# Optimization experiments

Hardware: AMD Instinct MI355X
Metric: run time of the kernel (lower is better)

The kernel has to match this reference:

```python
import jax, jax.numpy as jnp
import numpy as np
from jax import lax

T, H, L = 4096, 1024, 2  # seq_len, hidden (=input_dim), num_layers


def setup_inputs() -> dict:
    key = jax.random.key(0)
    ks = jax.random.split(key, 12)
    s = 1.0 / np.sqrt(H)
    u = lambda k, shp: jax.random.uniform(k, shp, jnp.float32, -s, s)
    return {
        "x": jax.random.normal(ks[0], (T, 1, H), jnp.float32),
        # encoder LSTM params, stacked over layers: W_ih/W_hh [L,4H,H], biases [L,4H]
        "enc_W_ih": u(ks[1], (L, 4 * H, H)),
        "enc_W_hh": u(ks[2], (L, 4 * H, H)),
        "enc_b_ih": u(ks[3], (L, 4 * H)),
        "enc_b_hh": u(ks[4], (L, 4 * H)),
        # decoder LSTM params
        "dec_W_ih": u(ks[5], (L, 4 * H, H)),
        "dec_W_hh": u(ks[6], (L, 4 * H, H)),
        "dec_b_ih": u(ks[7], (L, 4 * H)),
        "dec_b_hh": u(ks[8], (L, 4 * H)),
        # output Linear: H -> input_dim (=H)
        "out_W": u(ks[9], (H, H)),
        "out_b": u(ks[10], (H,)),
    }


def _lstm_layer(x_seq, W_ih, W_hh, b_ih, b_hh, h0, c0):
    """One LSTM layer over a full sequence. x_seq: [T,1,I]; returns hs [T,1,H], hT, cT [1,H].
    PyTorch gate order: i, f, g, o."""
    # precompute input contributions for all steps (one big GEMM)
    xg = jnp.einsum('tbi,gi->tbg', x_seq, W_ih) + b_ih  # [T,1,4H]

    def step(carry, xg_t):
        h, c = carry
        g = xg_t + h @ W_hh.T + b_hh  # [1,4H]
        i, f, gg, o = jnp.split(g, 4, axis=-1)
        c = jax.nn.sigmoid(f) * c + jax.nn.sigmoid(i) * jnp.tanh(gg)
        h = jax.nn.sigmoid(o) * jnp.tanh(c)
        return (h, c), h

    (hT, cT), hs = lax.scan(step, (h0, c0), xg)
    return hs, hT, cT


def reference(x, enc_W_ih, enc_W_hh, enc_b_ih, enc_b_hh,
              dec_W_ih, dec_W_hh, dec_b_ih, dec_b_hh, out_W, out_b):
    Tn = x.shape[0]
    nH = enc_W_hh.shape[-1]
    nL = enc_W_ih.shape[0]
    z = jnp.zeros((1, nH), x.dtype)

    # ---- encoder: stacked LSTM, layer-sequential (eval mode: no dropout) ----
    seq = x
    enc_h, enc_c = [], []
    for l in range(nL):
        seq, hT, cT = _lstm_layer(seq, enc_W_ih[l], enc_W_hh[l], enc_b_ih[l], enc_b_hh[l], z, z)
        enc_h.append(hT)
        enc_c.append(cT)

    final_hidden = seq[-1:]  # [1,1,H] = encoded_output[-1].unsqueeze(0)

    # ---- decoder: same constant input fed every step; init state = encoder (h,c) ----
    # The torch loop runs the full stacked LSTM one step at a time with constant input x;
    # stacked LSTMs are layer-separable, so we run each layer over all T steps at once.
    dseq = jnp.broadcast_to(final_hidden, (Tn, 1, nH))
    for l in range(nL):
        dseq, _, _ = _lstm_layer(dseq, dec_W_ih[l], dec_W_hh[l], dec_b_ih[l], dec_b_hh[l], enc_h[l], enc_c[l])

    out = jnp.einsum('tbh,oh->tbo', dseq, out_W) + out_b
    out = jnp.where(out > 0, out, 0.01 * out)  # LeakyReLU(0.01)
    reconstructed = jnp.flip(out, axis=0)  # decoded.reverse()
    return reconstructed, final_hidden
```

## Files before the change

kernel.cpp:

```cpp
#include <hip/hip_runtime.h>
#include <stdint.h>


#define T_STEPS 4096
#define H_DIM   1024
#define SLOT_U64 1024
#define SLOT_DW  2048
#define NSLOT   4097
#define M1 0x7E57u
#define M2 0x7E58u
#define PANIC_ITERS (1u<<25)

using u32 = uint32_t;
using u64 = unsigned long long;

static __device__ __forceinline__ float sigf(float x){ return 1.0f/(1.0f+__expf(-x)); }
static __device__ __forceinline__ float tanh_f(float x){
  x = fminf(20.f, fmaxf(-20.f, x));
  float e = __expf(-2.f*x);
  return (1.f-e)/(1.f+e);
}

static __device__ __forceinline__ bool tag_ok(u64 v, u32 magic){
  return ((((u32)(v>>16))&0xFFFFu)==magic) & (((u32)(v>>48))==magic);
}
static __device__ __forceinline__ float untag1(u64 v){
  return __uint_as_float( (((u32)v)&0xFFFFu) | (((u32)(v>>32))<<16) );
}
static __device__ __forceinline__ u64 tag1(u32 magic, float h){
  u32 b=__float_as_uint(h);
  u64 lo = (u64)((magic<<16)|(b&0xFFFFu));
  u64 hi = ((u64)((magic<<16)|(b>>16)))<<32;
  return hi|lo;
}

static __device__ __forceinline__ void poll_h2(const u64* __restrict__ q,
                                               u32 magic, float* dst,
                                               u32* panic){
  u64 v0=0,v1=0; bool ok0=false,ok1=false; u32 it=0;
  for(;;){
    if(!ok0) v0=__hip_atomic_load(q,  __ATOMIC_RELAXED,__HIP_MEMORY_SCOPE_AGENT);
    if(!ok1) v1=__hip_atomic_load(q+1,__ATOMIC_RELAXED,__HIP_MEMORY_SCOPE_AGENT);
    ok0 = ok0 || tag_ok(v0,magic);
    ok1 = ok1 || tag_ok(v1,magic);
    if(ok0 & ok1) break;
    ++it;
    if((it & 255u)==0u){
      if(__hip_atomic_load(panic,__ATOMIC_RELAXED,__HIP_MEMORY_SCOPE_AGENT)==0xDEADBEEFu) break;
      if(it>PANIC_ITERS){ __hip_atomic_store(panic,0xDEADBEEFu,__ATOMIC_RELAXED,__HIP_MEMORY_SCOPE_AGENT); break; }
    }
    __builtin_amdgcn_s_sleep(4);
  }
  dst[0]=untag1(v0);
  dst[1]=untag1(v1);
}

static __device__ __forceinline__ void poll_in2h2(const u64* __restrict__ qa, u32 mA,
                                                  const u64* __restrict__ qb, u32 mB,
                                                  float* da, float* db, u32* panic){
  u64 a0=0,a1=0,b0=0,b1=0; bool oa0=false,oa1=false,ob0=false,ob1=false; u32 it=0;
  for(;;){
    if(!oa0) a0=__hip_atomic_load(qa,  __ATOMIC_RELAXED,__HIP_MEMORY_SCOPE_AGENT);
    if(!oa1) a1=__hip_atomic_load(qa+1,__ATOMIC_RELAXED,__HIP_MEMORY_SCOPE_AGENT);
    if(!ob0) b0=__hip_atomic_load(qb,  __ATOMIC_RELAXED,__HIP_MEMORY_SCOPE_AGENT);
    if(!ob1) b1=__hip_atomic_load(qb+1,__ATOMIC_RELAXED,__HIP_MEMORY_SCOPE_AGENT);
    oa0 = oa0 || tag_ok(a0,mA);
    oa1 = oa1 || tag_ok(a1,mA);
    ob0 = ob0 || tag_ok(b0,mB);
    ob1 = ob1 || tag_ok(b1,mB);
    if(oa0 & oa1 & ob0 & ob1) break;
    ++it;
    if((it & 255u)==0u){
      if(__hip_atomic_load(panic,__ATOMIC_RELAXED,__HIP_MEMORY_SCOPE_AGENT)==0xDEADBEEFu) break;
      if(it>PANIC_ITERS){ __hip_atomic_store(panic,0xDEADBEEFu,__ATOMIC_RELAXED,__HIP_MEMORY_SCOPE_AGENT); break; }
    }
    __builtin_amdgcn_s_sleep(4);
  }
  da[0]=untag1(a0); da[1]=untag1(a1);
  db[0]=untag1(b0); db[1]=untag1(b1);
}

static __device__ __forceinline__ void lstm_scan_body(
    int kb, int tid, float* st, float* gl,
    const float* __restrict__ xin,
    const u64*  __restrict__ instream,
    u64*        __restrict__ own,
    u32 m_in, u32 m_own,
    const float* __restrict__ Wih, const float* __restrict__ Whh,
    const float* __restrict__ bih, const float* __restrict__ bhh,
    const float* __restrict__ c0,
    float*       __restrict__ cout,
    const u64*  __restrict__ h0slot,
    float*       __restrict__ fh_out,
    u32* __restrict__ panic,
    int mode)
{
  const int hr0=kb*8;
  const int w=tid>>6, l=tid&63;
  const int g=w>>1, q=w&1;
  const int grow0=(g<<10)+hr0+(q<<2);
  const int e0 = 2*tid;
  const int fb  = e0 + 4*(e0>>5);
  const int fbH = 1152+fb;
  const int sb  = l*36;

  float wr0[32],wr1[32],wr2[32],wr3[32];
  {
    const float* srcb = (l<32) ? Wih + (size_t)grow0*H_DIM + l*32
                               : Whh + (size_t)grow0*H_DIM + (l-32)*32;
    #pragma unroll
    for(int i=0;i<8;i++){
      float4 a0=*(const float4*)(srcb + i*4);
      float4 a1=*(const float4*)(srcb + 1024 + i*4);
      float4 a2=*(const float4*)(srcb + 2048 + i*4);
      float4 a3=*(const float4*)(srcb + 3072 + i*4);
      wr0[4*i]=a0.x; wr0[4*i+1]=a0.y; wr0[4*i+2]=a0.z; wr0[4*i+3]=a0.w;
      wr1[4*i]=a1.x; wr1[4*i+1]=a1.y; wr1[4*i+2]=a1.z; wr1[4*i+3]=a1.w;
      wr2[4*i]=a2.x; wr2[4*i+1]=a2.y; wr2[4*i+2]=a2.z; wr2[4*i+3]=a2.w;
      wr3[4*i]=a3.x; wr3[4*i+1]=a3.y; wr3[4*i+2]=a3.z; wr3[4*i+3]=a3.w;
    }
  }

  float bI=0,bF=0,bG=0,bO=0,c_st=0.f,h_st=0.f;
  if(tid<8){
    int o=hr0+tid;
    bI=bih[o]       + bhh[o];
    bF=bih[o+1024]  + bhh[o+1024];
    bG=bih[o+2048]  + bhh[o+2048];
    bO=bih[o+3072]  + bhh[o+3072];
    if(c0)     c_st=c0[o];
    if(h0slot) h_st=untag1(h0slot[o]);
    __hip_atomic_store(own+o, tag1(m_own,h_st), __ATOMIC_RELAXED,__HIP_MEMORY_SCOPE_AGENT);
  }
  if(mode==2){
    st[fb]  =untag1(instream[e0]);
    st[fb+1]=untag1(instream[e0+1]);
  }

  for(int t=0;t<T_STEPS;++t){
    if(mode==0){
      float2 xv=*(const float2*)(xin + (size_t)t*H_DIM + e0);
      st[fb]=xv.x; st[fb+1]=xv.y;
      poll_h2(own + (size_t)t*SLOT_U64 + e0, m_own, st+fbH, panic);
    } else if(mode==2){
      poll_h2(own + (size_t)t*SLOT_U64 + e0, m_own, st+fbH, panic);
    } else {
      poll_in2h2(instream + (size_t)(t+1)*SLOT_U64 + e0, m_in,
                 own      + (size_t)t*SLOT_U64     + e0, m_own,
                 st+fb, st+fbH, panic);
    }
    __syncthreads();
    float p0=0.f,p1=0.f,p2=0.f,p3=0.f;
    #pragma unroll
    for(int i=0;i<8;i++){
      float4 s=*(const float4*)(st+sb+i*4);
      p0+=s.x*wr0[4*i]+s.y*wr0[4*i+1]+s.z*wr0[4*i+2]+s.w*wr0[4*i+3];
      p1+=s.x*wr1[4*i]+s.y*wr1[4*i+1]+s.z*wr1[4*i+2]+s.w*wr1[4*i+3];
      p2+=s.x*wr2[4*i]+s.y*wr2[4*i+1]+s.z*wr2[4*i+2]+s.w*wr2[4*i+3];
      p3+=s.x*wr3[4*i]+s.y*wr3[4*i+1]+s.z*wr3[4*i+2]+s.w*wr3[4*i+3];
    }
    #pragma unroll
    for(int off=32;off;off>>=1){
      p0+=__shfl_down(p0,off,64); p1+=__shfl_down(p1,off,64);
      p2+=__shfl_down(p2,off,64); p3+=__shfl_down(p3,off,64);
    }
    if(l==0){ gl[w*4+0]=p0; gl[w*4+1]=p1; gl[w*4+2]=p2; gl[w*4+3]=p3; }
    __syncthreads();
    if(tid<8){
      float gi=bI+gl[tid], gf=bF+gl[8+tid], gg=bG+gl[16+tid], go=bO+gl[24+tid];
      c_st = sigf(gf)*c_st + sigf(gi)*tanh_f(gg);
      h_st = sigf(go)*tanh_f(c_st);
      __hip_atomic_store(own + (size_t)(t+1)*SLOT_U64 + hr0 + tid,
                         tag1(m_own,h_st), __ATOMIC_RELAXED,__HIP_MEMORY_SCOPE_AGENT);
      if(t==T_STEPS-1){
        cout[hr0+tid]=c_st;
        if(fh_out) fh_out[hr0+tid]=h_st;
      }
    }
  }
}

__global__ __launch_bounds__(512,2) void lstm_scan_pair(
    const float* __restrict__ xinA,
    const u64*  __restrict__ insA, u64* __restrict__ ownA, u32 miA, u32 moA,
    const float* __restrict__ WihA, const float* __restrict__ WhhA,
    const float* __restrict__ bihA, const float* __restrict__ bhhA,
    const float* __restrict__ c0A, float* __restrict__ coutA,
    const u64*  __restrict__ h0A, float* __restrict__ fhA, int modeA,
    const u64*  __restrict__ insB, u64* __restrict__ ownB, u32 miB, u32 moB,
    const float* __restrict__ WihB, const float* __restrict__ WhhB,
    const float* __restrict__ bihB, const float* __restrict__ bhhB,
    const float* __restrict__ c0B, float* __restrict__ coutB,
    const u64*  __restrict__ h0B, float* __restrict__ fhB, int modeB,
    u32* __restrict__ panic)
{
  __shared__ __align__(16) float st[2304];
  __shared__ float gl[32];
  const int b=blockIdx.x, tid=threadIdx.x;
  if(b<128){
    lstm_scan_body(b, tid, st, gl, xinA, insA, ownA, miA, moA,
                   WihA, WhhA, bihA, bhhA, c0A, coutA, h0A, fhA, panic, modeA);
  } else {
    lstm_scan_body(b-128, tid, st, gl, nullptr, insB, ownB, miB, moB,
                   WihB, WhhB, bihB, bhhB, c0B, coutB, h0B, fhB, panic, modeB);
  }
}

__global__ __launch_bounds__(256) void proj_out(
    const u64* __restrict__ SB, const float* __restrict__ oW,
    const float* __restrict__ ob, float* __restrict__ out)
{
  __shared__ __align__(16) float hb[1024];
  const int tp=blockIdx.x, tid=threadIdx.x;
  #pragma unroll
  for(int j=0;j<4;j++)
    hb[tid*4+j] = untag1(SB[(size_t)(tp+1)*SLOT_U64 + tid*4 + j]);
  __syncthreads();
  #pragma unroll
  for(int j=0;j<4;j++){
    int o = tid + 256*j;
    const float* wr = oW + (size_t)o*H_DIM;
    float acc=0.f;
    for(int k=0;k<1024;k+=4){
      float4 wv=*(const float4*)(wr+k);
      acc += wv.x*hb[k]+wv.y*hb[k+1]+wv.z*hb[k+2]+wv.w*hb[k+3];
    }
    acc += ob[o];
    acc = acc>0.f ? acc : 0.01f*acc;
    out[(size_t)(4095-tp)*H_DIM + o]=acc;
  }
}

extern "C" void kernel_launch(void* const* d_in, const int* in_sizes, int n_in,
                              void* d_out, int out_size, void* d_ws, size_t ws_size,
                              hipStream_t stream) {
  const float* x    = (const float*)d_in[0];
  const float* eWih = (const float*)d_in[1];
  const float* eWhh = (const float*)d_in[2];
  const float* ebih = (const float*)d_in[3];
  const float* ebhh = (const float*)d_in[4];
  const float* dWih = (const float*)d_in[5];
  const float* dWhh = (const float*)d_in[6];
  const float* dbih = (const float*)d_in[7];
  const float* dbhh = (const float*)d_in[8];
  const float* oW   = (const float*)d_in[9];
  const float* ob   = (const float*)d_in[10];
  float* out = (float*)d_out;
  u32* ws = (u32*)d_ws;

  const size_t REGION = (size_t)NSLOT*SLOT_DW;
  u64*   SA    = (u64*)ws;
  u64*   SB    = (u64*)(ws + REGION);
  float* CA    = (float*)(ws + 2*REGION);
  u32*   panic = ws + 2*REGION + 2048;
  const size_t LSTRIDE = (size_t)4096*1024;

  size_t clr_bytes = (2*REGION + 2048 + 64)*4;
  hipMemsetAsync(d_ws, 0, clr_bytes, stream);

  lstm_scan_pair<<<256,512,0,stream>>>(
      x, nullptr, SA, 0u, M1,
      eWih, eWhh, ebih, ebhh,
      nullptr, CA, nullptr, nullptr, 0,
      SA, SB, M1, M1,
      eWih+LSTRIDE, eWhh+LSTRIDE, ebih+4096, ebhh+4096,
      nullptr, CA+1024, nullptr, out + (size_t)T_STEPS*H_DIM, 1,
      panic);

  lstm_scan_pair<<<256,512,0,stream>>>(
      nullptr, SB + (size_t)4096*SLOT_U64, SA, 0u, M2,
      dWih, dWhh, dbih, dbhh,
      CA, CA, SA + (size_t)4096*SLOT_U64, nullptr, 2,
      SA, SB, M2, M2,
      dWih+LSTRIDE, dWhh+LSTRIDE, dbih+4096, dbhh+4096,
      CA+1024, CA+1024, SB + (size_t)4096*SLOT_U64, nullptr, 3,
      panic);

  proj_out<<<4096,256,0,stream>>>(SB, oW, ob, out);
}
```

Measured before the change: 25.27 ms.

## Replace tagged-value polling with per-block monotonic flags and plain h buffers

New measurement: 45.44 ms. 1.8x slower.

```diff
diff --git a/kernel.cpp b/kernel.cpp
--- a/kernel.cpp
+++ b/kernel.cpp
@@ -4,12 +4,9 @@
 
 #define T_STEPS 4096
 #define H_DIM   1024
-#define SLOT_U64 1024
-#define SLOT_DW  2048
 #define NSLOT   4097
-#define M1 0x7E57u
-#define M2 0x7E58u
-#define PANIC_ITERS (1u<<25)
+#define FLAG_STRIDE 16
+#define PANIC_ITERS (1u<<23)
 
 using u32 = uint32_t;
 using u64 = unsigned long long;
@@ -21,76 +18,43 @@
   return (1.f-e)/(1.f+e);
 }
 
-static __device__ __forceinline__ bool tag_ok(u64 v, u32 magic){
-  return ((((u32)(v>>16))&0xFFFFu)==magic) & (((u32)(v>>48))==magic);
-}
-static __device__ __forceinline__ float untag1(u64 v){
-  return __uint_as_float( (((u32)v)&0xFFFFu) | (((u32)(v>>32))<<16) );
-}
-static __device__ __forceinline__ u64 tag1(u32 magic, float h){
-  u32 b=__float_as_uint(h);
-  u64 lo = (u64)((magic<<16)|(b&0xFFFFu));
-  u64 hi = ((u64)((magic<<16)|(b>>16)))<<32;
-  return hi|lo;
-}
-
-static __device__ __forceinline__ void poll_h2(const u64* __restrict__ q,
-                                               u32 magic, float* dst,
-                                               u32* panic){
-  u64 v0=0,v1=0; bool ok0=false,ok1=false; u32 it=0;
-  for(;;){
-    if(!ok0) v0=__hip_atomic_load(q,  __ATOMIC_RELAXED,__HIP_MEMORY_SCOPE_AGENT);
-    if(!ok1) v1=__hip_atomic_load(q+1,__ATOMIC_RELAXED,__HIP_MEMORY_SCOPE_AGENT);
-    ok0 = ok0 || tag_ok(v0,magic);
-    ok1 = ok1 || tag_ok(v1,magic);
-    if(ok0 & ok1) break;
-    ++it;
-    if((it & 255u)==0u){
+static __device__ __forceinline__ u64 pk2(float a, float b){
+  return (u64)__float_as_uint(a) | (((u64)__float_as_uint(b))<<32);
+}
+static __device__ __forceinline__ void ld2a(const float* p, float* dst){
+  u64 v=__hip_atomic_load((const u64*)p,__ATOMIC_RELAXED,__HIP_MEMORY_SCOPE_AGENT);
+  dst[0]=__uint_as_float((u32)v);
+  dst[1]=__uint_as_float((u32)(v>>32));
+}
+static __device__ __forceinline__ float ld1a(const float* p){
+  u32 v=__hip_atomic_load((const u32*)p,__ATOMIC_RELAXED,__HIP_MEMORY_SCOPE_AGENT);
+  return __uint_as_float(v);
+}
+
+static __device__ __forceinline__ void poll_flag(const u32* __restrict__ f,
+                                                 u32 want, u32* panic){
+  u32 it=0;
+  while(__hip_atomic_load(f,__ATOMIC_RELAXED,__HIP_MEMORY_SCOPE_AGENT) < want){
+    if(((++it)&255u)==0u){
       if(__hip_atomic_load(panic,__ATOMIC_RELAXED,__HIP_MEMORY_SCOPE_AGENT)==0xDEADBEEFu) break;
       if(it>PANIC_ITERS){ __hip_atomic_store(panic,0xDEADBEEFu,__ATOMIC_RELAXED,__HIP_MEMORY_SCOPE_AGENT); break; }
-    }
-    __builtin_amdgcn_s_sleep(4);
-  }
-  dst[0]=untag1(v0);
-  dst[1]=untag1(v1);
-}
-
-static __device__ __forceinline__ void poll_in2h2(const u64* __restrict__ qa, u32 mA,
-                                                  const u64* __restrict__ qb, u32 mB,
-                                                  float* da, float* db, u32* panic){
-  u64 a0=0,a1=0,b0=0,b1=0; bool oa0=false,oa1=false,ob0=false,ob1=false; u32 it=0;
-  for(;;){
-    if(!oa0) a0=__hip_atomic_load(qa,  __ATOMIC_RELAXED,__HIP_MEMORY_SCOPE_AGENT);
-    if(!oa1) a1=__hip_atomic_load(qa+1,__ATOMIC_RELAXED,__HIP_MEMORY_SCOPE_AGENT);
-    if(!ob0) b0=__hip_atomic_load(qb,  __ATOMIC_RELAXED,__HIP_MEMORY_SCOPE_AGENT);
-    if(!ob1) b1=__hip_atomic_load(qb+1,__ATOMIC_RELAXED,__HIP_MEMORY_SCOPE_AGENT);
-    oa0 = oa0 || tag_ok(a0,mA);
-    oa1 = oa1 || tag_ok(a1,mA);
-    ob0 = ob0 || tag_ok(b0,mB);
-    ob1 = ob1 || tag_ok(b1,mB);
-    if(oa0 & oa1 & ob0 & ob1) break;
-    ++it;
-    if((it & 255u)==0u){
-      if(__hip_atomic_load(panic,__ATOMIC_RELAXED,__HIP_MEMORY_SCOPE_AGENT)==0xDEADBEEFu) break;
-      if(it>PANIC_ITERS){ __hip_atomic_store(panic,0xDEADBEEFu,__ATOMIC_RELAXED,__HIP_MEMORY_SCOPE_AGENT); break; }
-    }
-    __builtin_amdgcn_s_sleep(4);
-  }
-  da[0]=untag1(a0); da[1]=untag1(a1);
-  db[0]=untag1(b0); db[1]=untag1(b1);
+      __builtin_amdgcn_s_sleep(1);
+    }
+  }
 }
 
 static __device__ __forceinline__ void lstm_scan_body(
     int kb, int tid, float* st, float* gl,
     const float* __restrict__ xin,
-    const u64*  __restrict__ instream,
-    u64*        __restrict__ own,
-    u32 m_in, u32 m_own,
+    const float* __restrict__ instream,
+    float*       __restrict__ own,
+    const u32*  __restrict__ flagIn,
+    u32*        __restrict__ flagOwn,
     const float* __restrict__ Wih, const float* __restrict__ Whh,
     const float* __restrict__ bih, const float* __restrict__ bhh,
     const float* __restrict__ c0,
     float*       __restrict__ cout,
-    const u64*  __restrict__ h0slot,
+    const float* __restrict__ h0slot,
     float*       __restrict__ fh_out,
     u32* __restrict__ panic,
     int mode)
@@ -103,6 +67,8 @@
   const int fb  = e0 + 4*(e0>>5);
   const int fbH = 1152+fb;
   const int sb  = l*36;
+  u32* myflag = flagOwn + kb*FLAG_STRIDE;
+  const bool has_in = (mode==1)||(mode==3);
 
   float wr0[32],wr1[32],wr2[32],wr3[32];
   {
@@ -129,26 +95,40 @@
     bG=bih[o+2048]  + bhh[o+2048];
     bO=bih[o+3072]  + bhh[o+3072];
     if(c0)     c_st=c0[o];
-    if(h0slot) h_st=untag1(h0slot[o]);
-    __hip_atomic_store(own+o, tag1(m_own,h_st), __ATOMIC_RELAXED,__HIP_MEMORY_SCOPE_AGENT);
+    if(h0slot) h_st=ld1a(h0slot+o);
+  }
+  if(w==0){
+    float h0v=__shfl(h_st,0,64), h1v=__shfl(h_st,1,64);
+    float h2v=__shfl(h_st,2,64), h3v=__shfl(h_st,3,64);
+    float h4v=__shfl(h_st,4,64), h5v=__shfl(h_st,5,64);
+    float h6v=__shfl(h_st,6,64), h7v=__shfl(h_st,7,64);
+    if(l==0){
+      u64* dst=(u64*)(own + hr0);
+      __hip_atomic_store(dst+0, pk2(h0v,h1v), __ATOMIC_RELAXED,__HIP_MEMORY_SCOPE_AGENT);
+      __hip_atomic_store(dst+1, pk2(h2v,h3v), __ATOMIC_RELAXED,__HIP_MEMORY_SCOPE_AGENT);
+      __hip_atomic_store(dst+2, pk2(h4v,h5v), __ATOMIC_RELAXED,__HIP_MEMORY_SCOPE_AGENT);
+      __hip_atomic_store(dst+3, pk2(h6v,h7v), __ATOMIC_RELAXED,__HIP_MEMORY_SCOPE_AGENT);
+      __hip_atomic_store(myflag, 1u, __ATOMIC_RELEASE,__HIP_MEMORY_SCOPE_AGENT);
+    }
   }
   if(mode==2){
-    st[fb]  =untag1(instream[e0]);
-    st[fb+1]=untag1(instream[e0+1]);
+    ld2a(instream+e0, st+fb);
   }
 
   for(int t=0;t<T_STEPS;++t){
+    if(tid<128){
+      poll_flag(flagOwn + tid*FLAG_STRIDE, (u32)(t+1), panic);
+    } else if(has_in && tid<256){
+      poll_flag(flagIn + (tid-128)*FLAG_STRIDE, (u32)(t+2), panic);
+    }
+    __syncthreads();
     if(mode==0){
       float2 xv=*(const float2*)(xin + (size_t)t*H_DIM + e0);
       st[fb]=xv.x; st[fb+1]=xv.y;
-      poll_h2(own + (size_t)t*SLOT_U64 + e0, m_own, st+fbH, panic);
-    } else if(mode==2){
-      poll_h2(own + (size_t)t*SLOT_U64 + e0, m_own, st+fbH, panic);
-    } else {
-      poll_in2h2(instream + (size_t)(t+1)*SLOT_U64 + e0, m_in,
-                 own      + (size_t)t*SLOT_U64     + e0, m_own,
-                 st+fb, st+fbH, panic);
-    }
+    } else if(has_in){
+      ld2a(instream + (size_t)(t+1)*H_DIM + e0, st+fb);
+    }
+    ld2a(own + (size_t)t*H_DIM + e0, st+fbH);
     __syncthreads();
     float p0=0.f,p1=0.f,p2=0.f,p3=0.f;
     #pragma unroll
@@ -170,51 +150,64 @@
       float gi=bI+gl[tid], gf=bF+gl[8+tid], gg=bG+gl[16+tid], go=bO+gl[24+tid];
       c_st = sigf(gf)*c_st + sigf(gi)*tanh_f(gg);
       h_st = sigf(go)*tanh_f(c_st);
-      __hip_atomic_store(own + (size_t)(t+1)*SLOT_U64 + hr0 + tid,
-                         tag1(m_own,h_st), __ATOMIC_RELAXED,__HIP_MEMORY_SCOPE_AGENT);
       if(t==T_STEPS-1){
         cout[hr0+tid]=c_st;
         if(fh_out) fh_out[hr0+tid]=h_st;
       }
     }
+    if(w==0){
+      float h0v=__shfl(h_st,0,64), h1v=__shfl(h_st,1,64);
+      float h2v=__shfl(h_st,2,64), h3v=__shfl(h_st,3,64);
+      float h4v=__shfl(h_st,4,64), h5v=__shfl(h_st,5,64);
+      float h6v=__shfl(h_st,6,64), h7v=__shfl(h_st,7,64);
+      if(l==0){
+        u64* dst=(u64*)(own + (size_t)(t+1)*H_DIM + hr0);
+        __hip_atomic_store(dst+0, pk2(h0v,h1v), __ATOMIC_RELAXED,__HIP_MEMORY_SCOPE_AGENT);
+        __hip_atomic_store(dst+1, pk2(h2v,h3v), __ATOMIC_RELAXED,__HIP_MEMORY_SCOPE_AGENT);
+        __hip_atomic_store(dst+2, pk2(h4v,h5v), __ATOMIC_RELAXED,__HIP_MEMORY_SCOPE_AGENT);
+        __hip_atomic_store(dst+3, pk2(h6v,h7v), __ATOMIC_RELAXED,__HIP_MEMORY_SCOPE_AGENT);
+        __hip_atomic_store(myflag, (u32)(t+2), __ATOMIC_RELEASE,__HIP_MEMORY_SCOPE_AGENT);
+      }
+    }
   }
 }
 
 __global__ __launch_bounds__(512,2) void lstm_scan_pair(
     const float* __restrict__ xinA,
-    const u64*  __restrict__ insA, u64* __restrict__ ownA, u32 miA, u32 moA,
+    const float* __restrict__ insA, float* __restrict__ ownA,
+    const u32* __restrict__ fInA, u32* __restrict__ fOwnA,
     const float* __restrict__ WihA, const float* __restrict__ WhhA,
     const float* __restrict__ bihA, const float* __restrict__ bhhA,
     const float* __restrict__ c0A, float* __restrict__ coutA,
-    const u64*  __restrict__ h0A, float* __restrict__ fhA, int modeA,
-    const u64*  __restrict__ insB, u64* __restrict__ ownB, u32 miB, u32 moB,
+    const float* __restrict__ h0A, float* __restrict__ fhA, int modeA,
+    const float* __restrict__ insB, float* __restrict__ ownB,
+    const u32* __restrict__ fInB, u32* __restrict__ fOwnB,
     const float* __restrict__ WihB, const float* __restrict__ WhhB,
     const float* __restrict__ bihB, const float* __restrict__ bhhB,
     const float* __restrict__ c0B, float* __restrict__ coutB,
-    const u64*  __restrict__ h0B, float* __restrict__ fhB, int modeB,
+    const float* __restrict__ h0B, float* __restrict__ fhB, int modeB,
     u32* __restrict__ panic)
 {
   __shared__ __align__(16) float st[2304];
   __shared__ float gl[32];
   const int b=blockIdx.x, tid=threadIdx.x;
   if(b<128){
-    lstm_scan_body(b, tid, st, gl, xinA, insA, ownA, miA, moA,
+    lstm_scan_body(b, tid, st, gl, xinA, insA, ownA, fInA, fOwnA,
                    WihA, WhhA, bihA, bhhA, c0A, coutA, h0A, fhA, panic, modeA);
   } else {
-    lstm_scan_body(b-128, tid, st, gl, nullptr, insB, ownB, miB, moB,
+    lstm_scan_body(b-128, tid, st, gl, nullptr, insB, ownB, fInB, fOwnB,
                    WihB, WhhB, bihB, bhhB, c0B, coutB, h0B, fhB, panic, modeB);
   }
 }
 
 __global__ __launch_bounds__(256) void proj_out(
-    const u64* __restrict__ SB, const float* __restrict__ oW,
+    const float* __restrict__ SB, const float* __restrict__ oW,
     const float* __restrict__ ob, float* __restrict__ out)
 {
   __shared__ __align__(16) float hb[1024];
   const int tp=blockIdx.x, tid=threadIdx.x;
-  #pragma unroll
-  for(int j=0;j<4;j++)
-    hb[tid*4+j] = untag1(SB[(size_t)(tp+1)*SLOT_U64 + tid*4 + j]);
+  ld2a(SB + (size_t)(tp+1)*H_DIM + tid*4,     hb + tid*4);
+  ld2a(SB + (size_t)(tp+1)*H_DIM + tid*4 + 2, hb + tid*4 + 2);
   __syncthreads();
   #pragma unroll
   for(int j=0;j<4;j++){
@@ -248,32 +241,36 @@
   float* out = (float*)d_out;
   u32* ws = (u32*)d_ws;
 
-  const size_t REGION = (size_t)NSLOT*SLOT_DW;
-  u64*   SA    = (u64*)ws;
-  u64*   SB    = (u64*)(ws + REGION);
+  const size_t REGION = (size_t)NSLOT*H_DIM;
+  float* SA    = (float*)ws;
+  float* SB    = (float*)(ws + REGION);
   float* CA    = (float*)(ws + 2*REGION);
   u32*   panic = ws + 2*REGION + 2048;
+  u32*   F1A   = panic + 64;
+  u32*   F1B   = F1A + 128*FLAG_STRIDE;
+  u32*   F2A   = F1B + 128*FLAG_STRIDE;
+  u32*   F2B   = F2A + 128*FLAG_STRIDE;
   const size_t LSTRIDE = (size_t)4096*1024;
 
-  size_t clr_bytes = (2*REGION + 2048 + 64)*4;
-  hipMemsetAsync(d_ws, 0, clr_bytes, stream);
+  size_t clr_bytes = (2048 + 64 + 4*128*FLAG_STRIDE)*4;
+  hipMemsetAsync((void*)(ws + 2*REGION), 0, clr_bytes, stream);
 
   lstm_scan_pair<<<256,512,0,stream>>>(
-      x, nullptr, SA, 0u, M1,
+      x, nullptr, SA, nullptr, F1A,
       eWih, eWhh, ebih, ebhh,
       nullptr, CA, nullptr, nullptr, 0,
-      SA, SB, M1, M1,
+      SA, SB, F1A, F1B,
       eWih+LSTRIDE, eWhh+LSTRIDE, ebih+4096, ebhh+4096,
       nullptr, CA+1024, nullptr, out + (size_t)T_STEPS*H_DIM, 1,
       panic);
 
   lstm_scan_pair<<<256,512,0,stream>>>(
-      nullptr, SB + (size_t)4096*SLOT_U64, SA, 0u, M2,
+      nullptr, SB + (size_t)4096*H_DIM, SA, nullptr, F2A,
       dWih, dWhh, dbih, dbhh,
-      CA, CA, SA + (size_t)4096*SLOT_U64, nullptr, 2,
-      SA, SB, M2, M2,
+      CA, CA, SA + (size_t)4096*H_DIM, nullptr, 2,
+      SA, SB, F2A, F2B,
       dWih+LSTRIDE, dWhh+LSTRIDE, dbih+4096, dbhh+4096,
-      CA+1024, CA+1024, SB + (size_t)4096*SLOT_U64, nullptr, 3,
+      CA+1024, CA+1024, SB + (size_t)4096*H_DIM, nullptr, 3,
       panic);
 
   proj_out<<<4096,256,0,stream>>>(SB, oW, ob, out);
```
